# Performance work log

Measured on AMD Instinct MI355X. Metric: run time of the kernel, lower is better.

The kernel has to match this reference:

```python
import jax, jax.numpy as jnp
import numpy as np

B, T, C, H = 8, 2048, 1024, 128

def setup_inputs() -> dict:
    key = jax.random.key(0)
    kx, kq, kk, kv = jax.random.split(key, 4)
    x = jax.random.normal(kx, (B, T, C), dtype=jnp.float32)
    # torch nn.Linear(C, H, bias=False) computes x @ W.T with W of shape [H, C];
    # we store the transposed [C, H] matrices directly.
    Wq = jax.random.normal(kq, (C, H), dtype=jnp.float32) * (C ** -0.5)
    Wk = jax.random.normal(kk, (C, H), dtype=jnp.float32) * (C ** -0.5)
    Wv = jax.random.normal(kv, (C, H), dtype=jnp.float32) * (C ** -0.5)
    return {"x": x, "Wq": Wq, "Wk": Wk, "Wv": Wv}

def reference(x, Wq, Wk, Wv):
    # x: [B,T,C]; projections: [B,T,H]
    q = jnp.einsum('btc,ch->bth', x, Wq)
    k = jnp.einsum('btc,ch->bth', x, Wk)
    v = jnp.einsum('btc,ch->bth', x, Wv)
    scale = k.shape[-1] ** -0.5
    wei = jnp.einsum('bth,bsh->bts', q, k) * scale          # [B,T,T]
    # causal mask: position t attends to s <= t
    causal = jnp.tril(jnp.ones((x.shape[1], x.shape[1]), dtype=bool))
    wei = jnp.where(causal, wei, -jnp.inf)
    wei = jax.nn.softmax(wei, axis=-1)
    # dropout p=0.0 -> identity
    out = jnp.einsum('bts,bsh->bth', wei, v)                # [B,T,H]
    return out
```

## Files before the change

### kernel.cpp

```cpp
#include <hip/hip_runtime.h>
#include <hip/hip_bf16.h>

#define DB 8
#define DT 2048
#define DC 1024
#define DH 128

typedef __attribute__((ext_vector_type(8))) short short8;
typedef __attribute__((ext_vector_type(4))) float f32x4;
typedef __attribute__((ext_vector_type(4))) int i32x4;
typedef __attribute__((ext_vector_type(4))) unsigned short u16x4;

static __device__ __forceinline__ unsigned short bfbits(float x){
    union { float f; unsigned u; } a; a.f = x;
    unsigned u = a.u;
    unsigned r = u + 0x7fffu + ((u >> 16) & 1u);
    return (unsigned short)(r >> 16);
}
static __device__ __forceinline__ unsigned pbf2(float lo, float hi){
    return (unsigned)bfbits(lo) | ((unsigned)bfbits(hi) << 16);
}
static __device__ __forceinline__ float bf2f(unsigned short u){
    union { unsigned u; float f; } t; t.u = ((unsigned)u) << 16; return t.f;
}

static __device__ __forceinline__ void gload16(const void* g, void* l){
    __builtin_amdgcn_global_load_lds(
        (const __attribute__((address_space(1))) unsigned int*)g,
        (__attribute__((address_space(3))) unsigned int*)l, 16, 0, 0);
}

static __device__ __forceinline__ short8 redist(unsigned pk0, unsigned pk1,
                                                unsigned pk2, unsigned pk3,
                                                int g, int c){
    const int src0 = c + (((2*g    ) & 3) << 4);
    const int src1 = c + (((2*g + 1) & 3) << 4);
    const int sel  = g >> 1;
    unsigned a0 = __shfl(pk0, src0), a2 = __shfl(pk2, src0);
    unsigned b0 = __shfl(pk1, src0), b2 = __shfl(pk3, src0);
    unsigned c0 = __shfl(pk0, src1), c2 = __shfl(pk2, src1);
    unsigned d0 = __shfl(pk1, src1), d2 = __shfl(pk3, src1);
    i32x4 pw = { (int)(sel ? a2 : a0), (int)(sel ? b2 : b0),
                 (int)(sel ? c2 : c0), (int)(sel ? d2 : d0) };
    return __builtin_bit_cast(short8, pw);
}

__global__ __launch_bounds__(256) void prep_wt_kernel(const float* __restrict__ Wq,
                                                      const float* __restrict__ Wk,
                                                      const float* __restrict__ Wv,
                                                      unsigned short* __restrict__ WTc){
    int gid = blockIdx.x * 256 + threadIdx.x;
    int e  = gid & 7;
    int F3 = gid >> 3;
    int n  = F3 % 384;
    int ct = F3 / 384;
    int k  = (ct >> 2) * 32 + (ct & 3) * 8 + e;
    int p  = n >> 7, h = n & 127;
    const float* W = (p == 0) ? Wq : (p == 1 ? Wk : Wv);
    float v = W[(size_t)k * DH + h];
    if (p == 0) v *= 0.08838834764831845f * 1.4426950408889634f;
    WTc[gid] = bfbits(v);
}

__global__ __launch_bounds__(512, 2) void qkv_kernel(const float* __restrict__ x,
                                                     const unsigned short* __restrict__ WTc,
                                                     unsigned short* __restrict__ Qb,
                                                     unsigned short* __restrict__ Kb,
                                                     unsigned short* __restrict__ VT){
    __shared__ unsigned short Bs[2][24576];
    __shared__ unsigned short As[2][4608];

    const int tid  = threadIdx.x;
    const int lane = tid & 63;
    const int w    = tid >> 6;
    const int g = lane >> 4, c = lane & 15;
    const int m0 = blockIdx.x * 64;
    const int n0 = w * 48;

    const unsigned short* bsrc = WTc + (size_t)tid * 8;
    const int arow = tid >> 3, ac8 = tid & 7;
    const float* asrc = x + (size_t)(m0 + arow) * DC + ac8 * 8;

    f32x4 acc[4][3] = {};
    float4 av0, av1;

#pragma unroll
    for (int j = 0; j < 6; ++j)
        gload16(bsrc + j * 4096, &Bs[0][j * 4096 + tid * 8]);
    {
        av0 = *(const float4*)asrc; av1 = *(const float4*)(asrc + 4);
        i32x4 h8 = { (int)pbf2(av0.x, av0.y), (int)pbf2(av0.z, av0.w),
                     (int)pbf2(av1.x, av1.y), (int)pbf2(av1.z, av1.w) };
        *(i32x4*)(&As[0][arow * 72 + ac8 * 8]) = h8;
    }

    for (int t = 0; t < DC / 64; ++t){
        const int cur = t & 1;
        __syncthreads();
        if (t < DC / 64 - 1){
#pragma unroll
            for (int j = 0; j < 6; ++j)
                gload16(bsrc + (t + 1) * 24576 + j * 4096,
                        &Bs[cur ^ 1][j * 4096 + tid * 8]);
            av0 = *(const float4*)(asrc + (t + 1) * 64);
            av1 = *(const float4*)(asrc + (t + 1) * 64 + 4);
        }
#pragma unroll
        for (int kk = 0; kk < 2; ++kk){
            short8 af[4], bfr[3];
#pragma unroll
            for (int mf = 0; mf < 4; ++mf)
                af[mf] = *(const short8*)(&As[cur][(mf*16 + c) * 72 + kk*32 + g * 8]);
#pragma unroll
            for (int nf = 0; nf < 3; ++nf)
                bfr[nf] = *(const short8*)(&Bs[cur][kk*12288 + g * 3072 + (n0 + nf*16 + c) * 8]);
#pragma unroll
            for (int mf = 0; mf < 4; ++mf)
#pragma unroll
                for (int nf = 0; nf < 3; ++nf)
                    acc[mf][nf] = __builtin_amdgcn_mfma_f32_16x16x32_bf16(af[mf], bfr[nf], acc[mf][nf], 0, 0, 0);
        }
        if (t < DC / 64 - 1){
            i32x4 h8 = { (int)pbf2(av0.x, av0.y), (int)pbf2(av0.z, av0.w),
                         (int)pbf2(av1.x, av1.y), (int)pbf2(av1.z, av1.w) };
            *(i32x4*)(&As[cur ^ 1][arow * 72 + ac8 * 8]) = h8;
        }
    }

    const int bb = m0 >> 11;
    const int tb = m0 & 2047;
#pragma unroll
    for (int mf = 0; mf < 4; ++mf)
#pragma unroll
        for (int nf = 0; nf < 3; ++nf){
            const int n  = n0 + nf*16;
            const int p  = n >> 7;
            const int np = (n & 127) + c;
            const int row = m0 + mf*16 + 4*g;
            if (p < 2){
                unsigned short* O = (p == 0) ? Qb : Kb;
#pragma unroll
                for (int r = 0; r < 4; ++r)
                    O[(size_t)(row + r) * DH + np] = bfbits(acc[mf][nf][r]);
            } else {
                const int t0 = tb + mf*16 + 4*g;
                u16x4 v = { bfbits(acc[mf][nf][0]), bfbits(acc[mf][nf][1]),
                            bfbits(acc[mf][nf][2]), bfbits(acc[mf][nf][3]) };
                *(u16x4*)(VT + ((size_t)bb * DH + np) * DT + t0) = v;
            }
        }
}

__global__ __launch_bounds__(256, 2) void attn_kernel(const unsigned short* __restrict__ Qb,
                                                      const unsigned short* __restrict__ Kb,
                                                      const unsigned short* __restrict__ VT,
                                                      unsigned short* __restrict__ OP,
                                                      float* __restrict__ ML){
    __shared__ unsigned char lds[2][32768];

    const int tid  = threadIdx.x;
    const int lane = tid & 63;
    const int w    = tid >> 6;
    const int g = lane >> 4, c = lane & 15;
    const int bi = blockIdx.x;
    const int b  = bi & 7;
    const int idx = bi >> 3;
    const int qt   = (idx < 32) ? (31 - idx) : (idx - 32);
    const int half = idx >> 5;
    const int q0 = qt * 64;
    const int qw = q0 + 16 * w;
    const int q  = qw + c;
    const int nt = qt + 1;
    const int h1 = (nt + 1) >> 1;
    const int kt0 = half ? h1 : 0;
    const int kt1 = half ? nt : h1;

    const unsigned short* Kbase = Kb + (size_t)b * DT * DH;
    const unsigned short* Vbase = VT + (size_t)b * DH * DT;

    short8 qf[4];
#pragma unroll
    for (int hc = 0; hc < 4; ++hc)
        qf[hc] = *(const short8*)(Qb + ((size_t)b*DT + qw + c) * DH + hc*32 + g*8);

    f32x4 acc[8] = {};
    float m = -1e30f, l = 0.f;

    if (kt0 < kt1){
        {
            const int kv0 = kt0 * 64;
#pragma unroll
            for (int p = 0; p < 4; ++p){
                const int s = p*256 + tid;
                const int r = s >> 4, cbl = (s & 15) * 16;
                const int h = s >> 3, tbl = (s & 7) * 16;
                gload16(Kbase + (size_t)(kv0 + r) * DH + ((cbl ^ ((r & 7) << 4)) >> 1),
                        lds[0] + s*16);
                gload16(Vbase + (size_t)h * DT + kv0 + ((tbl ^ ((h & 7) << 4)) >> 1),
                        lds[0] + 16384 + s*16);
            }
        }

        for (int kt = kt0; kt < kt1; ++kt){
            const int cur = (kt - kt0) & 1;
            const int kv0c = kt * 64;
            __syncthreads();

            if (kt + 1 < kt1){
                const int nv0 = kv0c + 64;
#pragma unroll
                for (int p = 0; p < 4; ++p){
                    const int s = p*256 + tid;
                    const int r = s >> 4, cbl = (s & 15) * 16;
                    const int h = s >> 3, tbl = (s & 7) * 16;
                    gload16(Kbase + (size_t)(nv0 + r) * DH + ((cbl ^ ((r & 7) << 4)) >> 1),
                            lds[cur ^ 1] + s*16);
                    gload16(Vbase + (size_t)h * DT + nv0 + ((tbl ^ ((h & 7) << 4)) >> 1),
                            lds[cur ^ 1] + 16384 + s*16);
                }
            }

            const unsigned char* kb = lds[cur];
            const unsigned char* vb = lds[cur] + 16384;

            f32x4 s4[4] = {};
            short8 kf[4][4];
#pragma unroll
            for (int j = 0; j < 4; ++j){
                const int r = 16*j + c;
#pragma unroll
                for (int hc = 0; hc < 4; ++hc)
                    kf[j][hc] = *(const short8*)(kb + r*256 + ((hc*64 + g*16) ^ ((r & 7) << 4)));
            }
            __builtin_amdgcn_s_setprio(1);
#pragma unroll
            for (int hc = 0; hc < 4; ++hc)
#pragma unroll
                for (int j = 0; j < 4; ++j)
                    s4[j] = __builtin_amdgcn_mfma_f32_16x16x32_bf16(kf[j][hc], qf[hc], s4[j], 0,0,0);
            __builtin_amdgcn_s_setprio(0);

            if (kt == nt - 1){
#pragma unroll
                for (int j = 0; j < 4; ++j){
                    const int o = kv0c + 16*j + 4*g;
#pragma unroll
                    for (int r = 0; r < 4; ++r)
                        if (o + r > q) s4[j][r] = -1e30f;
                }
            }

            float tm = -1e30f;
#pragma unroll
            for (int j = 0; j < 4; ++j)
#pragma unroll
                for (int r = 0; r < 4; ++r) tm = fmaxf(tm, s4[j][r]);
            tm = fmaxf(tm, __shfl_xor(tm, 16));
            tm = fmaxf(tm, __shfl_xor(tm, 32));
            if (!__all(tm <= m + 8.f)){
                const float mn = fmaxf(m, tm);
                const float rs = exp2f(m - mn);
                l *= rs;
#pragma unroll
                for (int mt = 0; mt < 8; ++mt) acc[mt] *= rs;
                m = mn;
            }
            float p[4][4]; float ps = 0.f;
#pragma unroll
            for (int j = 0; j < 4; ++j)
#pragma unroll
                for (int r = 0; r < 4; ++r){
                    p[j][r] = exp2f(s4[j][r] - m);
                    ps += p[j][r];
                }
            ps += __shfl_xor(ps, 16);
            ps += __shfl_xor(ps, 32);
            l += ps;

            short8 pf0 = redist(pbf2(p[0][0], p[0][1]), pbf2(p[0][2], p[0][3]),
                                pbf2(p[1][0], p[1][1]), pbf2(p[1][2], p[1][3]), g, c);
            short8 pf1 = redist(pbf2(p[2][0], p[2][1]), pbf2(p[2][2], p[2][3]),
                                pbf2(p[3][0], p[3][1]), pbf2(p[3][2], p[3][3]), g, c);

#pragma unroll
            for (int kk = 0; kk < 2; ++kk){
                short8 vf[8];
#pragma unroll
                for (int mt = 0; mt < 8; ++mt){
                    const int h = mt*16 + c;
                    vf[mt] = *(const short8*)(vb + h*128 + ((kk*64 + g*16) ^ ((h & 7) << 4)));
                }
                const short8 pf = kk ? pf1 : pf0;
                __builtin_amdgcn_s_setprio(1);
#pragma unroll
                for (int mt = 0; mt < 8; ++mt)
                    acc[mt] = __builtin_amdgcn_mfma_f32_16x16x32_bf16(vf[mt], pf, acc[mt], 0,0,0);
                __builtin_amdgcn_s_setprio(0);
            }
        }
    }

    const size_t blk = ((size_t)(b * 32 + qt) * 2 + half);
    unsigned short* op = OP + blk * 8192;
    const int row = 16*w + c;
#pragma unroll
    for (int mt = 0; mt < 8; ++mt){
        u16x4 h = { bfbits(acc[mt][0]), bfbits(acc[mt][1]),
                    bfbits(acc[mt][2]), bfbits(acc[mt][3]) };
        *(u16x4*)(op + row*128 + mt*16 + 4*g) = h;
    }
    if (g == 0){
        ML[(blk*64 + row)*2    ] = m;
        ML[(blk*64 + row)*2 + 1] = l;
    }
}

__global__ __launch_bounds__(256) void merge_kernel(const unsigned short* __restrict__ OP,
                                                    const float* __restrict__ ML,
                                                    float* __restrict__ out){
    const int tid = threadIdx.x;
    const int r  = tid >> 2;
    const int cq = (tid & 3) * 32;
    const int bi = blockIdx.x;
    const int b  = bi & 7;
    const int qt = bi >> 3;
    const size_t blk = (size_t)(b * 32 + qt) * 2;

    float ms[2], ls[2];
#pragma unroll
    for (int s = 0; s < 2; ++s){
        ms[s] = ML[((blk + s)*64 + r)*2    ];
        ls[s] = ML[((blk + s)*64 + r)*2 + 1];
    }
    const float M = fmaxf(ms[0], ms[1]);
    float sc[2]; float L = 0.f;
#pragma unroll
    for (int s = 0; s < 2; ++s){ sc[s] = exp2f(ms[s] - M); L += ls[s] * sc[s]; }
    const float inv = 1.0f / L;

    float* orow = out + ((size_t)(b * DT + qt*64 + r)) * DH + cq;
#pragma unroll
    for (int j = 0; j < 4; ++j){
        float o[8] = {};
#pragma unroll
        for (int s = 0; s < 2; ++s){
            short8 v = *(const short8*)(OP + (blk + s)*8192 + r*128 + cq + j*8);
#pragma unroll
            for (int e = 0; e < 8; ++e)
                o[e] += bf2f((unsigned short)v[e]) * sc[s];
        }
        f32x4 o0 = { o[0]*inv, o[1]*inv, o[2]*inv, o[3]*inv };
        f32x4 o1 = { o[4]*inv, o[5]*inv, o[6]*inv, o[7]*inv };
        *(f32x4*)(orow + j*8    ) = o0;
        *(f32x4*)(orow + j*8 + 4) = o1;
    }
}

extern "C" void kernel_launch(void* const* d_in, const int* in_sizes, int n_in,
                              void* d_out, int out_size, void* d_ws, size_t ws_size,
                              hipStream_t stream){
    const float* x  = (const float*)d_in[0];
    const float* Wq = (const float*)d_in[1];
    const float* Wk = (const float*)d_in[2];
    const float* Wv = (const float*)d_in[3];
    float* out = (float*)d_out;

    unsigned short* WTc = (unsigned short*)d_ws;
    unsigned short* Qb = WTc + 3 * DH * DC;
    unsigned short* Kb = Qb + (size_t)DB * DT * DH;
    unsigned short* VT = Kb + (size_t)DB * DT * DH;
    unsigned short* OP = VT + (size_t)DB * DT * DH;
    float*          ML = (float*)(OP + (size_t)512 * 8192);

    hipLaunchKernelGGL(prep_wt_kernel, dim3(1536), dim3(256), 0, stream, Wq, Wk, Wv, WTc);
    hipLaunchKernelGGL(qkv_kernel, dim3(256), dim3(512), 0, stream, x, WTc, Qb, Kb, VT);
    hipLaunchKernelGGL(attn_kernel, dim3(512), dim3(256), 0, stream, Qb, Kb, VT, OP, ML);
    hipLaunchKernelGGL(merge_kernel, dim3(256), dim3(256), 0, stream, OP, ML, out);
}
```

Measured before the change: 74.19 us.

## Process 128-query tiles per block with two row groups per wave and four-way KV split

Each attention block now covers 128 queries instead of 64. Each wave holds two 16-row Q fragments and two sets of accumulators, so every K/V tile staged in LDS feeds twice as many MFMAs. The causal KV range is split four ways instead of two to keep 512 blocks. Waves whose rows all lie before the current KV tile skip its compute. The merge kernel now combines four partials per row, which doubles the partial-output workspace and raises register pressure per wave.

```diff
diff --git a/kernel.cpp b/kernel.cpp
--- a/kernel.cpp
+++ b/kernel.cpp
@@ -165,39 +165,40 @@
     const int bi = blockIdx.x;
     const int b  = bi & 7;
     const int idx = bi >> 3;
-    const int qt   = (idx < 32) ? (31 - idx) : (idx - 32);
-    const int half = idx >> 5;
-    const int q0 = qt * 64;
-    const int qw = q0 + 16 * w;
-    const int q  = qw + c;
-    const int nt = qt + 1;
-    const int h1 = (nt + 1) >> 1;
-    const int kt0 = half ? h1 : 0;
-    const int kt1 = half ? nt : h1;
+    const int qt  = idx & 15;
+    const int s   = idx >> 4;
+    const int base0 = qt * 128 + w * 32;
+    const int q0v = base0 + c;
+    const int q1v = base0 + 16 + c;
+    const int nt  = 2 * (qt + 1);
+    const int kt0 = (nt * s) >> 2;
+    const int kt1 = (nt * (s + 1)) >> 2;
 
     const unsigned short* Kbase = Kb + (size_t)b * DT * DH;
     const unsigned short* Vbase = VT + (size_t)b * DH * DT;
 
-    short8 qf[4];
-#pragma unroll
-    for (int hc = 0; hc < 4; ++hc)
-        qf[hc] = *(const short8*)(Qb + ((size_t)b*DT + qw + c) * DH + hc*32 + g*8);
-
-    f32x4 acc[8] = {};
-    float m = -1e30f, l = 0.f;
+    short8 qf0[4], qf1[4];
+#pragma unroll
+    for (int hc = 0; hc < 4; ++hc){
+        qf0[hc] = *(const short8*)(Qb + ((size_t)b*DT + base0 + c) * DH + hc*32 + g*8);
+        qf1[hc] = *(const short8*)(Qb + ((size_t)b*DT + base0 + 16 + c) * DH + hc*32 + g*8);
+    }
+
+    f32x4 acc0[8] = {}, acc1[8] = {};
+    float m0 = -1e30f, l0 = 0.f, m1 = -1e30f, l1 = 0.f;
 
     if (kt0 < kt1){
         {
             const int kv0 = kt0 * 64;
 #pragma unroll
             for (int p = 0; p < 4; ++p){
-                const int s = p*256 + tid;
-                const int r = s >> 4, cbl = (s & 15) * 16;
-                const int h = s >> 3, tbl = (s & 7) * 16;
+                const int sfl = p*256 + tid;
+                const int r = sfl >> 4, cbl = (sfl & 15) * 16;
+                const int h = sfl >> 3, tbl = (sfl & 7) * 16;
                 gload16(Kbase + (size_t)(kv0 + r) * DH + ((cbl ^ ((r & 7) << 4)) >> 1),
-                        lds[0] + s*16);
+                        lds[0] + sfl*16);
                 gload16(Vbase + (size_t)h * DT + kv0 + ((tbl ^ ((h & 7) << 4)) >> 1),
-                        lds[0] + 16384 + s*16);
+                        lds[0] + 16384 + sfl*16);
             }
         }
 
@@ -210,108 +211,139 @@
                 const int nv0 = kv0c + 64;
 #pragma unroll
                 for (int p = 0; p < 4; ++p){
-                    const int s = p*256 + tid;
-                    const int r = s >> 4, cbl = (s & 15) * 16;
-                    const int h = s >> 3, tbl = (s & 7) * 16;
+                    const int sfl = p*256 + tid;
+                    const int r = sfl >> 4, cbl = (sfl & 15) * 16;
+                    const int h = sfl >> 3, tbl = (sfl & 7) * 16;
                     gload16(Kbase + (size_t)(nv0 + r) * DH + ((cbl ^ ((r & 7) << 4)) >> 1),
-                            lds[cur ^ 1] + s*16);
+                            lds[cur ^ 1] + sfl*16);
                     gload16(Vbase + (size_t)h * DT + nv0 + ((tbl ^ ((h & 7) << 4)) >> 1),
-                            lds[cur ^ 1] + 16384 + s*16);
+                            lds[cur ^ 1] + 16384 + sfl*16);
                 }
             }
 
-            const unsigned char* kb = lds[cur];
-            const unsigned char* vb = lds[cur] + 16384;
-
-            f32x4 s4[4] = {};
-            short8 kf[4][4];
-#pragma unroll
-            for (int j = 0; j < 4; ++j){
-                const int r = 16*j + c;
+            if (kv0c <= base0){
+                const unsigned char* kb = lds[cur];
+                const unsigned char* vb = lds[cur] + 16384;
+
+                f32x4 s40[4] = {}, s41[4] = {};
+                short8 kf[4][4];
+#pragma unroll
+                for (int j = 0; j < 4; ++j){
+                    const int r = 16*j + c;
+#pragma unroll
+                    for (int hc = 0; hc < 4; ++hc)
+                        kf[j][hc] = *(const short8*)(kb + r*256 + ((hc*64 + g*16) ^ ((r & 7) << 4)));
+                }
+                __builtin_amdgcn_s_setprio(1);
 #pragma unroll
                 for (int hc = 0; hc < 4; ++hc)
-                    kf[j][hc] = *(const short8*)(kb + r*256 + ((hc*64 + g*16) ^ ((r & 7) << 4)));
+#pragma unroll
+                    for (int j = 0; j < 4; ++j){
+                        s40[j] = __builtin_amdgcn_mfma_f32_16x16x32_bf16(kf[j][hc], qf0[hc], s40[j], 0,0,0);
+                        s41[j] = __builtin_amdgcn_mfma_f32_16x16x32_bf16(kf[j][hc], qf1[hc], s41[j], 0,0,0);
+                    }
+                __builtin_amdgcn_s_setprio(0);
+
+                if (kv0c + 63 > base0){
+#pragma unroll
+                    for (int j = 0; j < 4; ++j){
+                        const int o = kv0c + 16*j + 4*g;
+#pragma unroll
+                        for (int r = 0; r < 4; ++r){
+                            if (o + r > q0v) s40[j][r] = -1e30f;
+                            if (o + r > q1v) s41[j][r] = -1e30f;
+                        }
+                    }
+                }
+
+                float tm0 = -1e30f, tm1 = -1e30f;
+#pragma unroll
+                for (int j = 0; j < 4; ++j)
+#pragma unroll
+                    for (int r = 0; r < 4; ++r){
+                        tm0 = fmaxf(tm0, s40[j][r]);
+                        tm1 = fmaxf(tm1, s41[j][r]);
+                    }
+                tm0 = fmaxf(tm0, __shfl_xor(tm0, 16));
+                tm0 = fmaxf(tm0, __shfl_xor(tm0, 32));
+                tm1 = fmaxf(tm1, __shfl_xor(tm1, 16));
+                tm1 = fmaxf(tm1, __shfl_xor(tm1, 32));
+                if (!__all(tm0 <= m0 + 8.f)){
+                    const float mn = fmaxf(m0, tm0);
+                    const float rs = exp2f(m0 - mn);
+                    l0 *= rs;
+#pragma unroll
+                    for (int mt = 0; mt < 8; ++mt) acc0[mt] *= rs;
+                    m0 = mn;
+                }
+                if (!__all(tm1 <= m1 + 8.f)){
+                    const float mn = fmaxf(m1, tm1);
+                    const float rs = exp2f(m1 - mn);
+                    l1 *= rs;
+#pragma unroll
+                    for (int mt = 0; mt < 8; ++mt) acc1[mt] *= rs;
+                    m1 = mn;
+                }
+                float p0[4][4], p1[4][4]; float ps0 = 0.f, ps1 = 0.f;
+#pragma unroll
+                for (int j = 0; j < 4; ++j)
+#pragma unroll
+                    for (int r = 0; r < 4; ++r){
+                        p0[j][r] = exp2f(s40[j][r] - m0); ps0 += p0[j][r];
+                        p1[j][r] = exp2f(s41[j][r] - m1); ps1 += p1[j][r];
+                    }
+                ps0 += __shfl_xor(ps0, 16); ps0 += __shfl_xor(ps0, 32); l0 += ps0;
+                ps1 += __shfl_xor(ps1, 16); ps1 += __shfl_xor(ps1, 32); l1 += ps1;
+
+                short8 pf0a = redist(pbf2(p0[0][0], p0[0][1]), pbf2(p0[0][2], p0[0][3]),
+                                     pbf2(p0[1][0], p0[1][1]), pbf2(p0[1][2], p0[1][3]), g, c);
+                short8 pf0b = redist(pbf2(p0[2][0], p0[2][1]), pbf2(p0[2][2], p0[2][3]),
+                                     pbf2(p0[3][0], p0[3][1]), pbf2(p0[3][2], p0[3][3]), g, c);
+                short8 pf1a = redist(pbf2(p1[0][0], p1[0][1]), pbf2(p1[0][2], p1[0][3]),
+                                     pbf2(p1[1][0], p1[1][1]), pbf2(p1[1][2], p1[1][3]), g, c);
+                short8 pf1b = redist(pbf2(p1[2][0], p1[2][1]), pbf2(p1[2][2], p1[2][3]),
+                                     pbf2(p1[3][0], p1[3][1]), pbf2(p1[3][2], p1[3][3]), g, c);
+
+#pragma unroll
+                for (int kk = 0; kk < 2; ++kk){
+                    short8 vf[8];
+#pragma unroll
+                    for (int mt = 0; mt < 8; ++mt){
+                        const int h = mt*16 + c;
+                        vf[mt] = *(const short8*)(vb + h*128 + ((kk*64 + g*16) ^ ((h & 7) << 4)));
+                    }
+                    const short8 pfa = kk ? pf0b : pf0a;
+                    const short8 pfb = kk ? pf1b : pf1a;
+                    __builtin_amdgcn_s_setprio(1);
+#pragma unroll
+                    for (int mt = 0; mt < 8; ++mt){
+                        acc0[mt] = __builtin_amdgcn_mfma_f32_16x16x32_bf16(vf[mt], pfa, acc0[mt], 0,0,0);
+                        acc1[mt] = __builtin_amdgcn_mfma_f32_16x16x32_bf16(vf[mt], pfb, acc1[mt], 0,0,0);
+                    }
+                    __builtin_amdgcn_s_setprio(0);
+                }
             }
-            __builtin_amdgcn_s_setprio(1);
-#pragma unroll
-            for (int hc = 0; hc < 4; ++hc)
-#pragma unroll
-                for (int j = 0; j < 4; ++j)
-                    s4[j] = __builtin_amdgcn_mfma_f32_16x16x32_bf16(kf[j][hc], qf[hc], s4[j], 0,0,0);
-            __builtin_amdgcn_s_setprio(0);
-
-            if (kt == nt - 1){
-#pragma unroll
-                for (int j = 0; j < 4; ++j){
-                    const int o = kv0c + 16*j + 4*g;
-#pragma unroll
-                    for (int r = 0; r < 4; ++r)
-                        if (o + r > q) s4[j][r] = -1e30f;
-                }
-            }
-
-            float tm = -1e30f;
-#pragma unroll
-            for (int j = 0; j < 4; ++j)
-#pragma unroll
-                for (int r = 0; r < 4; ++r) tm = fmaxf(tm, s4[j][r]);
-            tm = fmaxf(tm, __shfl_xor(tm, 16));
-            tm = fmaxf(tm, __shfl_xor(tm, 32));
-            if (!__all(tm <= m + 8.f)){
-                const float mn = fmaxf(m, tm);
-                const float rs = exp2f(m - mn);
-                l *= rs;
-#pragma unroll
-                for (int mt = 0; mt < 8; ++mt) acc[mt] *= rs;
-                m = mn;
-            }
-            float p[4][4]; float ps = 0.f;
-#pragma unroll
-            for (int j = 0; j < 4; ++j)
-#pragma unroll
-                for (int r = 0; r < 4; ++r){
-                    p[j][r] = exp2f(s4[j][r] - m);
-                    ps += p[j][r];
-                }
-            ps += __shfl_xor(ps, 16);
-            ps += __shfl_xor(ps, 32);
-            l += ps;
-
-            short8 pf0 = redist(pbf2(p[0][0], p[0][1]), pbf2(p[0][2], p[0][3]),
-                                pbf2(p[1][0], p[1][1]), pbf2(p[1][2], p[1][3]), g, c);
-            short8 pf1 = redist(pbf2(p[2][0], p[2][1]), pbf2(p[2][2], p[2][3]),
-                                pbf2(p[3][0], p[3][1]), pbf2(p[3][2], p[3][3]), g, c);
-
-#pragma unroll
-            for (int kk = 0; kk < 2; ++kk){
-                short8 vf[8];
-#pragma unroll
-                for (int mt = 0; mt < 8; ++mt){
-                    const int h = mt*16 + c;
-                    vf[mt] = *(const short8*)(vb + h*128 + ((kk*64 + g*16) ^ ((h & 7) << 4)));
-                }
-                const short8 pf = kk ? pf1 : pf0;
-                __builtin_amdgcn_s_setprio(1);
-#pragma unroll
-                for (int mt = 0; mt < 8; ++mt)
-                    acc[mt] = __builtin_amdgcn_mfma_f32_16x16x32_bf16(vf[mt], pf, acc[mt], 0,0,0);
-                __builtin_amdgcn_s_setprio(0);
-            }
-        }
-    }
-
-    const size_t blk = ((size_t)(b * 32 + qt) * 2 + half);
-    unsigned short* op = OP + blk * 8192;
-    const int row = 16*w + c;
+        }
+    }
+
+    const size_t blk = (size_t)((b * 16 + qt) * 4 + s);
+    unsigned short* op = OP + blk * 16384;
+    const int row0 = w*32 + c;
+    const int row1 = row0 + 16;
 #pragma unroll
     for (int mt = 0; mt < 8; ++mt){
-        u16x4 h = { bfbits(acc[mt][0]), bfbits(acc[mt][1]),
-                    bfbits(acc[mt][2]), bfbits(acc[mt][3]) };
-        *(u16x4*)(op + row*128 + mt*16 + 4*g) = h;
+        u16x4 h0 = { bfbits(acc0[mt][0]), bfbits(acc0[mt][1]),
+                     bfbits(acc0[mt][2]), bfbits(acc0[mt][3]) };
+        u16x4 h1 = { bfbits(acc1[mt][0]), bfbits(acc1[mt][1]),
+                     bfbits(acc1[mt][2]), bfbits(acc1[mt][3]) };
+        *(u16x4*)(op + row0*128 + mt*16 + 4*g) = h0;
+        *(u16x4*)(op + row1*128 + mt*16 + 4*g) = h1;
     }
     if (g == 0){
-        ML[(blk*64 + row)*2    ] = m;
-        ML[(blk*64 + row)*2 + 1] = l;
+        ML[(blk*128 + row0)*2    ] = m0;
+        ML[(blk*128 + row0)*2 + 1] = l0;
+        ML[(blk*128 + row1)*2    ] = m1;
+        ML[(blk*128 + row1)*2 + 1] = l1;
     }
 }
 
@@ -319,32 +351,32 @@
                                                     const float* __restrict__ ML,
                                                     float* __restrict__ out){
     const int tid = threadIdx.x;
-    const int r  = tid >> 2;
-    const int cq = (tid & 3) * 32;
+    const int r  = tid >> 1;
     const int bi = blockIdx.x;
     const int b  = bi & 7;
-    const int qt = bi >> 3;
-    const size_t blk = (size_t)(b * 32 + qt) * 2;
-
-    float ms[2], ls[2];
-#pragma unroll
-    for (int s = 0; s < 2; ++s){
-        ms[s] = ML[((blk + s)*64 + r)*2    ];
-        ls[s] = ML[((blk + s)*64 + r)*2 + 1];
-    }
-    const float M = fmaxf(ms[0], ms[1]);
-    float sc[2]; float L = 0.f;
-#pragma unroll
-    for (int s = 0; s < 2; ++s){ sc[s] = exp2f(ms[s] - M); L += ls[s] * sc[s]; }
+    const int qt = (bi >> 3) & 15;
+    const int ch = (bi >> 7) * 64 + (tid & 1) * 32;
+    const size_t blk = (size_t)(b * 16 + qt) * 4;
+
+    float ms[4], ls[4];
+#pragma unroll
+    for (int s = 0; s < 4; ++s){
+        ms[s] = ML[((blk + s)*128 + r)*2    ];
+        ls[s] = ML[((blk + s)*128 + r)*2 + 1];
+    }
+    float M = fmaxf(fmaxf(ms[0], ms[1]), fmaxf(ms[2], ms[3]));
+    float sc[4]; float L = 0.f;
+#pragma unroll
+    for (int s = 0; s < 4; ++s){ sc[s] = exp2f(ms[s] - M); L += ls[s] * sc[s]; }
     const float inv = 1.0f / L;
 
-    float* orow = out + ((size_t)(b * DT + qt*64 + r)) * DH + cq;
+    float* orow = out + ((size_t)(b * DT + qt*128 + r)) * DH + ch;
 #pragma unroll
     for (int j = 0; j < 4; ++j){
         float o[8] = {};
 #pragma unroll
-        for (int s = 0; s < 2; ++s){
-            short8 v = *(const short8*)(OP + (blk + s)*8192 + r*128 + cq + j*8);
+        for (int s = 0; s < 4; ++s){
+            short8 v = *(const short8*)(OP + (blk + s)*16384 + r*128 + ch + j*8);
 #pragma unroll
             for (int e = 0; e < 8; ++e)
                 o[e] += bf2f((unsigned short)v[e]) * sc[s];
@@ -370,7 +402,7 @@
     unsigned short* Kb = Qb + (size_t)DB * DT * DH;
     unsigned short* VT = Kb + (size_t)DB * DT * DH;
     unsigned short* OP = VT + (size_t)DB * DT * DH;
-    float*          ML = (float*)(OP + (size_t)512 * 8192);
+    float*          ML = (float*)(OP + (size_t)512 * 16384);
 
     hipLaunchKernelGGL(prep_wt_kernel, dim3(1536), dim3(256), 0, stream, Wq, Wk, Wv, WTc);
     hipLaunchKernelGGL(qkv_kernel, dim3(256), dim3(512), 0, stream, x, WTc, Qb, Kb, VT);
```

Result: slower. 81.87 us (+10.3%).
